# Kernel optimization log

Hardware: AMD Instinct MI355X
Metric: run time of the kernel (lower is better)

Reference implementation:

```python
import jax, jax.numpy as jnp
import numpy as np

TAU = 2.0        # spikingjelly LIFNode default
V_TH = 1.0       # default v_threshold
V_RESET = 0.0    # default v_reset (hard reset)


def setup_inputs() -> dict:
    key = jax.random.key(0)
    k1, k2, k3 = jax.random.split(key, 3)
    T, B, N, Cin, Cout = 4, 8, 1024, 512, 512
    x = jax.random.normal(k1, (T, B, N, Cin), dtype=jnp.float32)
    # nn.Linear weights are [out, in]; kaiming-uniform-ish scale
    W1 = jax.random.normal(k2, (Cout, Cin), dtype=jnp.float32) / np.sqrt(Cin)
    W2 = jax.random.normal(k3, (Cout, Cout), dtype=jnp.float32) / np.sqrt(Cout)
    return {"x": x, "W1": W1, "W2": W2}


def _spike(v):
    # forward heaviside (ATan surrogate only matters for backward)
    return (v >= V_TH).astype(v.dtype)


def _lif_multistep(h):
    # h: [T, B, N, C]; multi-step LIF with decay_input=True, hard reset to 0
    v0 = jnp.zeros(h.shape[1:], dtype=h.dtype)

    def step(v, x_t):
        v = v + (x_t - (v - V_RESET)) / TAU   # leaky integration
        s = _spike(v)                          # threshold
        v = v * (1.0 - s) + V_RESET * s        # hard reset
        return v, s

    _, spikes = jax.lax.scan(step, v0, h)
    return spikes  # [T, B, N, C]


def reference(x, W1, W2):
    h = jnp.einsum('tbni,oi->tbno', x, W1)      # Linear(in_ch, out_ch, bias=False)
    s = _lif_multistep(h)                        # LIFNode, step_mode='m'
    out = jnp.einsum('tbno,po->tbnp', s, W2)    # Linear(out_ch, out_ch, bias=False)
    return out.astype(jnp.float32)
```

## Files before the change

### kernel.cpp

```cpp
#include <hip/hip_runtime.h>


typedef _Float16 half8  __attribute__((ext_vector_type(8)));
typedef _Float16 half4v __attribute__((ext_vector_type(4)));
typedef float    f32x4  __attribute__((ext_vector_type(4)));

constexpr int TT   = 4;
constexpr int BB   = 8;
constexpr int NN   = 1024;
constexpr int CC   = 512;
constexpr int MROW = BB * NN;
constexpr int MTOT = TT * MROW;
constexpr int BNC  = MROW * CC;
constexpr int LDK  = 40;
constexpr int LTA  = 140;
constexpr int LTB  = 284;

__device__ __forceinline__ int PADI(int r) { return r + ((r >> 5) << 2); }

__global__ __launch_bounds__(256)
void gemm1_chain3(const float* __restrict__ X, const float* __restrict__ W,
                  float* __restrict__ H) {
#pragma clang fp contract(off)
    __shared__ float At[32][LTA];
    __shared__ float Bt[32][LTB];

    const int tid = threadIdx.x;
    const int RM  = blockIdx.x * 128;
    const int CN  = blockIdx.y * 256;
    const int tx  = tid & 15;
    const int ty  = tid >> 4;
    const int abase = PADI(ty * 8);
    const int bbase = PADI(tx * 16);
    const int rot   = tid & 3;

    float acc[8][16] = {};

    for (int k0 = 0; k0 < CC; k0 += 32) {
        __syncthreads();
#pragma unroll
        for (int j = 0; j < 4; ++j) {
            int id  = tid + 256 * j;
            int row = id >> 3;
            int c4  = (id & 7) * 4;
            f32x4 v = *(const f32x4*)&X[(size_t)(RM + row) * CC + k0 + c4];
            int pr  = PADI(row);
#pragma unroll
            for (int e = 0; e < 4; ++e) {
                int ee = (e + rot) & 3;
                At[c4 + ee][pr] = v[ee];
            }
        }
#pragma unroll
        for (int j = 0; j < 8; ++j) {
            int id  = tid + 256 * j;
            int row = id >> 3;
            int c4  = (id & 7) * 4;
            f32x4 v = *(const f32x4*)&W[(size_t)(CN + row) * CC + k0 + c4];
            int pr  = PADI(row);
#pragma unroll
            for (int e = 0; e < 4; ++e) {
                int ee = (e + rot) & 3;
                Bt[c4 + ee][pr] = v[ee];
            }
        }
        __syncthreads();

#pragma unroll 2
        for (int k = 0; k < 32; ++k) {
            f32x4 a0 = *(const f32x4*)&At[k][abase];
            f32x4 a1 = *(const f32x4*)&At[k][abase + 4];
            f32x4 b0 = *(const f32x4*)&Bt[k][bbase];
            f32x4 b1 = *(const f32x4*)&Bt[k][bbase + 4];
            f32x4 b2 = *(const f32x4*)&Bt[k][bbase + 8];
            f32x4 b3 = *(const f32x4*)&Bt[k][bbase + 12];
            float a[8]  = {a0[0], a0[1], a0[2], a0[3], a1[0], a1[1], a1[2], a1[3]};
            float b[16] = {b0[0], b0[1], b0[2], b0[3], b1[0], b1[1], b1[2], b1[3],
                           b2[0], b2[1], b2[2], b2[3], b3[0], b3[1], b3[2], b3[3]};
#pragma unroll
            for (int i = 0; i < 8; ++i)
#pragma unroll
                for (int jj = 0; jj < 16; ++jj)
                    acc[i][jj] = __builtin_fmaf(a[i], b[jj], acc[i][jj]);
        }
    }

#pragma unroll
    for (int i = 0; i < 8; ++i) {
        size_t base = (size_t)(RM + ty * 8 + i) * CC + CN + tx * 16;
#pragma unroll
        for (int q = 0; q < 4; ++q) {
            f32x4 o = {acc[i][q * 4], acc[i][q * 4 + 1],
                       acc[i][q * 4 + 2], acc[i][q * 4 + 3]};
            *(f32x4*)&H[base + q * 4] = o;
        }
    }
}

__global__ __launch_bounds__(256)
void lif_np(const float* __restrict__ H, _Float16* __restrict__ S) {
#pragma clang fp contract(off)
    int g = blockIdx.x * 256 + threadIdx.x;
    float v[4] = {0.f, 0.f, 0.f, 0.f};
#pragma unroll
    for (int t = 0; t < TT; ++t) {
        f32x4 h = *(const f32x4*)&H[(size_t)t * BNC + (size_t)g * 4];
        half4v s;
#pragma unroll
        for (int e = 0; e < 4; ++e) {
            float d  = h[e] - v[e];
            float d2 = d * 0.5f;
            v[e] = v[e] + d2;
            bool sp = v[e] >= 1.0f;
            s[e] = sp ? (_Float16)1.0f : (_Float16)0.0f;
            if (sp) v[e] = 0.0f;
        }
        *(half4v*)&S[(size_t)t * BNC + (size_t)g * 4] = s;
    }
}

__global__ __launch_bounds__(256)
void gemm2_f16(const _Float16* __restrict__ S, const float* __restrict__ W,
               float* __restrict__ O) {
    __shared__ _Float16 As[128][LDK], Bs[128][LDK];

    const int tid  = threadIdx.x;
    const int RM   = blockIdx.x * 128;
    const int CN   = blockIdx.y * 128;
    const int lane = tid & 63;
    const int wv   = tid >> 6;
    const int wr   = (wv >> 1) * 64;
    const int wc   = (wv & 1) * 64;
    const int r15  = lane & 15;
    const int kg   = lane >> 4;

    f32x4 acc[4][4] = {};

    for (int k0 = 0; k0 < CC; k0 += 32) {
        __syncthreads();
#pragma unroll
        for (int j = 0; j < 2; ++j) {
            int id  = tid + 256 * j;
            int row = id >> 2;
            int c8  = (id & 3) * 8;
            *(half8*)&As[row][c8] =
                *(const half8*)&S[(size_t)(RM + row) * CC + k0 + c8];
        }
#pragma unroll
        for (int j = 0; j < 4; ++j) {
            int id  = tid + 256 * j;
            int row = id >> 3;
            int c4  = (id & 7) * 4;
            f32x4 v = *(const f32x4*)&W[(size_t)(CN + row) * CC + k0 + c4];
            half4v hv;
#pragma unroll
            for (int e = 0; e < 4; ++e) hv[e] = (_Float16)v[e];
            *(half4v*)&Bs[row][c4] = hv;
        }
        __syncthreads();

        half8 a[4], b[4];
#pragma unroll
        for (int i = 0; i < 4; ++i) {
            a[i] = *(const half8*)&As[wr + i * 16 + r15][kg * 8];
            b[i] = *(const half8*)&Bs[wc + i * 16 + r15][kg * 8];
        }
#pragma unroll
        for (int i = 0; i < 4; ++i)
#pragma unroll
            for (int j = 0; j < 4; ++j)
                acc[i][j] = __builtin_amdgcn_mfma_f32_16x16x32_f16(a[i], b[j], acc[i][j], 0, 0, 0);
    }

#pragma unroll
    for (int i = 0; i < 4; ++i)
#pragma unroll
        for (int j = 0; j < 4; ++j)
#pragma unroll
            for (int r = 0; r < 4; ++r) {
                int gm = RM + wr + i * 16 + kg * 4 + r;
                int gn = CN + wc + j * 16 + r15;
                O[(size_t)gm * CC + gn] = acc[i][j][r];
            }
}

extern "C" void kernel_launch(void* const* d_in, const int* in_sizes, int n_in,
                              void* d_out, int out_size, void* d_ws, size_t ws_size,
                              hipStream_t stream) {
    const float* x  = (const float*)d_in[0];
    const float* W1 = (const float*)d_in[1];
    const float* W2 = (const float*)d_in[2];
    float* out = (float*)d_out;

    float*    h = out;
    _Float16* s = (_Float16*)d_ws;

    dim3 g1(MTOT / 128, CC / 256);
    gemm1_chain3<<<g1, 256, 0, stream>>>(x, W1, h);

    lif_np<<<BNC / 4 / 256, 256, 0, stream>>>(h, s);

    dim3 g2(MTOT / 128, CC / 128);
    gemm2_f16<<<g2, 256, 0, stream>>>(s, W2, out);
}
```

Baseline: 271.1 us.

## Enlarge FP32 GEMM1 tile to 256x256 with double-buffered LDS and register prefetch

Grows the first GEMM's block tile from 128x256 to 256x256, so each thread accumulates a 16x16 output block. Global loads for the next-but-one K tile are prefetched into registers, and LDS is double-buffered so staging overlaps compute. The aim is more FLOPs per LDS byte and hidden global-memory latency. In exchange it needs 256 accumulator registers plus prefetch registers, forcing one block per CU (launch bounds 256,1) with likely register spills. The grid also halves to 512 blocks, which lowers occupancy and latency hiding.

```diff
diff --git a/kernel.cpp b/kernel.cpp
--- a/kernel.cpp
+++ b/kernel.cpp
@@ -13,81 +13,111 @@
 constexpr int MTOT = TT * MROW;
 constexpr int BNC  = MROW * CC;
 constexpr int LDK  = 40;
-constexpr int LTA  = 140;
-constexpr int LTB  = 284;
+constexpr int LTA3 = 284;
 
 __device__ __forceinline__ int PADI(int r) { return r + ((r >> 5) << 2); }
 
-__global__ __launch_bounds__(256)
-void gemm1_chain3(const float* __restrict__ X, const float* __restrict__ W,
+__global__ __launch_bounds__(256, 1)
+void gemm1_chain4(const float* __restrict__ X, const float* __restrict__ W,
                   float* __restrict__ H) {
 #pragma clang fp contract(off)
-    __shared__ float At[32][LTA];
-    __shared__ float Bt[32][LTB];
+    __shared__ float At[2][32][LTA3];
+    __shared__ float Bt[2][32][LTA3];
 
     const int tid = threadIdx.x;
-    const int RM  = blockIdx.x * 128;
+    const int RM  = blockIdx.x * 256;
     const int CN  = blockIdx.y * 256;
     const int tx  = tid & 15;
     const int ty  = tid >> 4;
-    const int abase = PADI(ty * 8);
+    const int abase = PADI(ty * 16);
     const int bbase = PADI(tx * 16);
-    const int rot   = tid & 3;
-
-    float acc[8][16] = {};
-
-    for (int k0 = 0; k0 < CC; k0 += 32) {
-        __syncthreads();
-#pragma unroll
-        for (int j = 0; j < 4; ++j) {
-            int id  = tid + 256 * j;
-            int row = id >> 3;
-            int c4  = (id & 7) * 4;
-            f32x4 v = *(const f32x4*)&X[(size_t)(RM + row) * CC + k0 + c4];
-            int pr  = PADI(row);
-#pragma unroll
-            for (int e = 0; e < 4; ++e) {
-                int ee = (e + rot) & 3;
-                At[c4 + ee][pr] = v[ee];
+    const int rot = tid & 3;
+
+    const int srow = tid >> 3;
+    const int sc4  = (tid & 7) * 4;
+    const int spr0 = PADI(srow);
+
+    float acc[16][16] = {};
+    f32x4 ra[8], rb[8];
+
+#pragma unroll
+    for (int j = 0; j < 8; ++j) {
+        size_t ro = (size_t)(RM + srow + 32 * j) * CC + sc4;
+        size_t co = (size_t)(CN + srow + 32 * j) * CC + sc4;
+        ra[j] = *(const f32x4*)&X[ro];
+        rb[j] = *(const f32x4*)&W[co];
+    }
+#pragma unroll
+    for (int j = 0; j < 8; ++j) {
+        int pr = spr0 + 36 * j;
+#pragma unroll
+        for (int e = 0; e < 4; ++e) {
+            int ee = (e + rot) & 3;
+            At[0][sc4 + ee][pr] = ra[j][ee];
+            Bt[0][sc4 + ee][pr] = rb[j][ee];
+        }
+    }
+#pragma unroll
+    for (int j = 0; j < 8; ++j) {
+        size_t ro = (size_t)(RM + srow + 32 * j) * CC + 32 + sc4;
+        size_t co = (size_t)(CN + srow + 32 * j) * CC + 32 + sc4;
+        ra[j] = *(const f32x4*)&X[ro];
+        rb[j] = *(const f32x4*)&W[co];
+    }
+    __syncthreads();
+
+    for (int kt = 0; kt < 16; ++kt) {
+        const int cur = kt & 1;
+        if (kt < 15) {
+#pragma unroll
+            for (int j = 0; j < 8; ++j) {
+                int pr = spr0 + 36 * j;
+#pragma unroll
+                for (int e = 0; e < 4; ++e) {
+                    int ee = (e + rot) & 3;
+                    At[cur ^ 1][sc4 + ee][pr] = ra[j][ee];
+                    Bt[cur ^ 1][sc4 + ee][pr] = rb[j][ee];
+                }
             }
         }
-#pragma unroll
-        for (int j = 0; j < 8; ++j) {
-            int id  = tid + 256 * j;
-            int row = id >> 3;
-            int c4  = (id & 7) * 4;
-            f32x4 v = *(const f32x4*)&W[(size_t)(CN + row) * CC + k0 + c4];
-            int pr  = PADI(row);
-#pragma unroll
-            for (int e = 0; e < 4; ++e) {
-                int ee = (e + rot) & 3;
-                Bt[c4 + ee][pr] = v[ee];
+        if (kt < 14) {
+            int kk = (kt + 2) * 32;
+#pragma unroll
+            for (int j = 0; j < 8; ++j) {
+                size_t ro = (size_t)(RM + srow + 32 * j) * CC + kk + sc4;
+                size_t co = (size_t)(CN + srow + 32 * j) * CC + kk + sc4;
+                ra[j] = *(const f32x4*)&X[ro];
+                rb[j] = *(const f32x4*)&W[co];
             }
         }
-        __syncthreads();
-
-#pragma unroll 2
+        const float (*Ac)[LTA3] = At[cur];
+        const float (*Bc)[LTA3] = Bt[cur];
+#pragma unroll 1
         for (int k = 0; k < 32; ++k) {
-            f32x4 a0 = *(const f32x4*)&At[k][abase];
-            f32x4 a1 = *(const f32x4*)&At[k][abase + 4];
-            f32x4 b0 = *(const f32x4*)&Bt[k][bbase];
-            f32x4 b1 = *(const f32x4*)&Bt[k][bbase + 4];
-            f32x4 b2 = *(const f32x4*)&Bt[k][bbase + 8];
-            f32x4 b3 = *(const f32x4*)&Bt[k][bbase + 12];
-            float a[8]  = {a0[0], a0[1], a0[2], a0[3], a1[0], a1[1], a1[2], a1[3]};
+            f32x4 a0 = *(const f32x4*)&Ac[k][abase];
+            f32x4 a1 = *(const f32x4*)&Ac[k][abase + 4];
+            f32x4 a2 = *(const f32x4*)&Ac[k][abase + 8];
+            f32x4 a3 = *(const f32x4*)&Ac[k][abase + 12];
+            f32x4 b0 = *(const f32x4*)&Bc[k][bbase];
+            f32x4 b1 = *(const f32x4*)&Bc[k][bbase + 4];
+            f32x4 b2 = *(const f32x4*)&Bc[k][bbase + 8];
+            f32x4 b3 = *(const f32x4*)&Bc[k][bbase + 12];
+            float a[16] = {a0[0], a0[1], a0[2], a0[3], a1[0], a1[1], a1[2], a1[3],
+                           a2[0], a2[1], a2[2], a2[3], a3[0], a3[1], a3[2], a3[3]};
             float b[16] = {b0[0], b0[1], b0[2], b0[3], b1[0], b1[1], b1[2], b1[3],
                            b2[0], b2[1], b2[2], b2[3], b3[0], b3[1], b3[2], b3[3]};
 #pragma unroll
-            for (int i = 0; i < 8; ++i)
+            for (int i = 0; i < 16; ++i)
 #pragma unroll
                 for (int jj = 0; jj < 16; ++jj)
                     acc[i][jj] = __builtin_fmaf(a[i], b[jj], acc[i][jj]);
         }
-    }
-
-#pragma unroll
-    for (int i = 0; i < 8; ++i) {
-        size_t base = (size_t)(RM + ty * 8 + i) * CC + CN + tx * 16;
+        __syncthreads();
+    }
+
+#pragma unroll
+    for (int i = 0; i < 16; ++i) {
+        size_t base = (size_t)(RM + ty * 16 + i) * CC + CN + tx * 16;
 #pragma unroll
         for (int q = 0; q < 4; ++q) {
             f32x4 o = {acc[i][q * 4], acc[i][q * 4 + 1],
@@ -195,8 +225,8 @@
     float*    h = out;
     _Float16* s = (_Float16*)d_ws;
 
-    dim3 g1(MTOT / 128, CC / 256);
-    gemm1_chain3<<<g1, 256, 0, stream>>>(x, W1, h);
+    dim3 g1(MTOT / 256, CC / 256);
+    gemm1_chain4<<<g1, 256, 0, stream>>>(x, W1, h);
 
     lif_np<<<BNC / 4 / 256, 256, 0, stream>>>(h, s);
 
```

Measured after the change: 366.9 us. 1.35x slower.

## Register-prefetch next K tile in gemm1 to overlap global loads with FMA

Applied to the files above, without the earlier changes.

The fp32 gemm1 kernel now loads the next K slice of X and W1 into registers while the current LDS tile is being consumed, and writes it to LDS after the compute loop. The goal is to hide global memory latency behind the FMA inner loop. It also sets launch_bounds to (256,2) to target two blocks per CU. The cost is 48 more prefetch registers on top of a 128-float accumulator, which the occupancy hint may force into spills.

```diff
diff --git a/kernel.cpp b/kernel.cpp
--- a/kernel.cpp
+++ b/kernel.cpp
@@ -18,8 +18,8 @@
 
 __device__ __forceinline__ int PADI(int r) { return r + ((r >> 5) << 2); }
 
-__global__ __launch_bounds__(256)
-void gemm1_chain3(const float* __restrict__ X, const float* __restrict__ W,
+__global__ __launch_bounds__(256, 2)
+void gemm1_chain5(const float* __restrict__ X, const float* __restrict__ W,
                   float* __restrict__ H) {
 #pragma clang fp contract(off)
     __shared__ float At[32][LTA];
@@ -34,38 +34,48 @@
     const int bbase = PADI(tx * 16);
     const int rot   = tid & 3;
 
+    const int arow = tid >> 3;
+    const int ac4  = (tid & 7) * 4;
+    const int brow = tid >> 3;
+    const int bc4  = (tid & 7) * 4;
+
     float acc[8][16] = {};
-
-    for (int k0 = 0; k0 < CC; k0 += 32) {
-        __syncthreads();
-#pragma unroll
-        for (int j = 0; j < 4; ++j) {
-            int id  = tid + 256 * j;
-            int row = id >> 3;
-            int c4  = (id & 7) * 4;
-            f32x4 v = *(const f32x4*)&X[(size_t)(RM + row) * CC + k0 + c4];
-            int pr  = PADI(row);
-#pragma unroll
-            for (int e = 0; e < 4; ++e) {
-                int ee = (e + rot) & 3;
-                At[c4 + ee][pr] = v[ee];
-            }
-        }
-#pragma unroll
-        for (int j = 0; j < 8; ++j) {
-            int id  = tid + 256 * j;
-            int row = id >> 3;
-            int c4  = (id & 7) * 4;
-            f32x4 v = *(const f32x4*)&W[(size_t)(CN + row) * CC + k0 + c4];
-            int pr  = PADI(row);
-#pragma unroll
-            for (int e = 0; e < 4; ++e) {
-                int ee = (e + rot) & 3;
-                Bt[c4 + ee][pr] = v[ee];
-            }
-        }
-        __syncthreads();
-
+    f32x4 ra[4], rb[8];
+
+#pragma unroll
+    for (int j = 0; j < 4; ++j)
+        ra[j] = *(const f32x4*)&X[(size_t)(RM + arow + 32 * j) * CC + ac4];
+#pragma unroll
+    for (int j = 0; j < 8; ++j)
+        rb[j] = *(const f32x4*)&W[(size_t)(CN + brow + 32 * j) * CC + bc4];
+
+#pragma unroll
+    for (int j = 0; j < 4; ++j) {
+        int pr = PADI(arow + 32 * j);
+#pragma unroll
+        for (int e = 0; e < 4; ++e) {
+            int ee = (e + rot) & 3;
+            At[ac4 + ee][pr] = ra[j][ee];
+        }
+    }
+#pragma unroll
+    for (int j = 0; j < 8; ++j) {
+        int pr = PADI(brow + 32 * j);
+#pragma unroll
+        for (int e = 0; e < 4; ++e) {
+            int ee = (e + rot) & 3;
+            Bt[bc4 + ee][pr] = rb[j][ee];
+        }
+    }
+#pragma unroll
+    for (int j = 0; j < 4; ++j)
+        ra[j] = *(const f32x4*)&X[(size_t)(RM + arow + 32 * j) * CC + 32 + ac4];
+#pragma unroll
+    for (int j = 0; j < 8; ++j)
+        rb[j] = *(const f32x4*)&W[(size_t)(CN + brow + 32 * j) * CC + 32 + bc4];
+    __syncthreads();
+
+    for (int kt = 0; kt < 16; ++kt) {
 #pragma unroll 2
         for (int k = 0; k < 32; ++k) {
             f32x4 a0 = *(const f32x4*)&At[k][abase];
@@ -83,6 +93,38 @@
                 for (int jj = 0; jj < 16; ++jj)
                     acc[i][jj] = __builtin_fmaf(a[i], b[jj], acc[i][jj]);
         }
+
+        if (kt < 15) {
+            __syncthreads();
+#pragma unroll
+            for (int j = 0; j < 4; ++j) {
+                int pr = PADI(arow + 32 * j);
+#pragma unroll
+                for (int e = 0; e < 4; ++e) {
+                    int ee = (e + rot) & 3;
+                    At[ac4 + ee][pr] = ra[j][ee];
+                }
+            }
+#pragma unroll
+            for (int j = 0; j < 8; ++j) {
+                int pr = PADI(brow + 32 * j);
+#pragma unroll
+                for (int e = 0; e < 4; ++e) {
+                    int ee = (e + rot) & 3;
+                    Bt[bc4 + ee][pr] = rb[j][ee];
+                }
+            }
+            if (kt < 14) {
+                int kk = (kt + 2) * 32;
+#pragma unroll
+                for (int j = 0; j < 4; ++j)
+                    ra[j] = *(const f32x4*)&X[(size_t)(RM + arow + 32 * j) * CC + kk + ac4];
+#pragma unroll
+                for (int j = 0; j < 8; ++j)
+                    rb[j] = *(const f32x4*)&W[(size_t)(CN + brow + 32 * j) * CC + kk + bc4];
+            }
+            __syncthreads();
+        }
     }
 
 #pragma unroll
@@ -196,7 +238,7 @@
     _Float16* s = (_Float16*)d_ws;
 
     dim3 g1(MTOT / 128, CC / 256);
-    gemm1_chain3<<<g1, 256, 0, stream>>>(x, W1, h);
+    gemm1_chain5<<<g1, 256, 0, stream>>>(x, W1, h);
 
     lif_np<<<BNC / 4 / 256, 256, 0, stream>>>(h, s);
 
```

New measurement: 280.6 us. 1.04x slower.
